# Performance work log

Hardware: AMD Instinct MI355X
Metric: run time of the kernel (lower is better)

Reference implementation:

```python
import jax, jax.numpy as jnp
import numpy as np

N = 50000
E = 800000
F_IN = 500
ID_DIM = 128
HID = 128
N_CLS = 40


def _init_linear(key, fan_in, fan_out, bias=True):
    k1, k2 = jax.random.split(key)
    bound = 1.0 / np.sqrt(fan_in)
    W = jax.random.uniform(k1, (fan_in, fan_out), minval=-bound, maxval=bound, dtype=jnp.float32)
    if bias:
        b = jax.random.uniform(k2, (fan_out,), minval=-bound, maxval=bound, dtype=jnp.float32)
        return W, b
    return W, None


def setup_inputs() -> dict:
    key = jax.random.key(0)
    ks = jax.random.split(key, 10)
    x = jax.random.normal(ks[0], (N, F_IN), dtype=jnp.float32)
    edge_index = jax.random.randint(ks[1], (2, E), 0, N, dtype=jnp.int32)
    W_map, b_map = _init_linear(ks[2], F_IN, ID_DIM)
    Wl1, bl1 = _init_linear(ks[3], ID_DIM, HID)
    Wr1, _ = _init_linear(ks[4], ID_DIM, HID, bias=False)
    Wl2, bl2 = _init_linear(ks[5], HID, 2 * HID)
    Wr2, _ = _init_linear(ks[6], HID, 2 * HID, bias=False)
    Wl3, bl3 = _init_linear(ks[7], 2 * HID, N_CLS)
    Wr3, _ = _init_linear(ks[8], 2 * HID, N_CLS, bias=False)
    return {"x": x, "edge_index": edge_index,
            "W_map": W_map, "b_map": b_map,
            "Wl1": Wl1, "bl1": bl1, "Wr1": Wr1,
            "Wl2": Wl2, "bl2": bl2, "Wr2": Wr2,
            "Wl3": Wl3, "bl3": bl3, "Wr3": Wr3}


def _sage_conv(x, src, dst, Wl, bl, Wr):
    # mean aggregation of source features into destination nodes
    agg = jax.ops.segment_sum(x[src], dst, num_segments=N)  # [N, d]
    cnt = jax.ops.segment_sum(jnp.ones((src.shape[0],), x.dtype), dst, num_segments=N)
    mean = agg / jnp.maximum(cnt, 1.0)[:, None]
    # SAGEConv (normalize=False): lin_l(mean_neigh) + lin_r(x), bias only on lin_l
    return mean @ Wl + bl + x @ Wr


def reference(x, edge_index, W_map, b_map, Wl1, bl1, Wr1, Wl2, bl2, Wr2, Wl3, bl3, Wr3):
    src, dst = edge_index[0], edge_index[1]
    h = x @ W_map + b_map                      # [N, 128]
    h = jax.nn.relu(_sage_conv(h, src, dst, Wl1, bl1, Wr1))   # dropout is identity in eval
    h = jax.nn.relu(_sage_conv(h, src, dst, Wl2, bl2, Wr2))
    h = _sage_conv(h, src, dst, Wl3, bl3, Wr3)
    return jax.nn.log_softmax(h, axis=1)
```

## Files before the change

### kernel.cpp

```cpp
#include <hip/hip_runtime.h>
#include <math.h>

#define NN 50000
#define NE 800000
#define FIN 500
#define NCLS 40
#define NB 196
#define G0 391
#define CNTB 1563
#define WSE 192512

typedef short short8 __attribute__((ext_vector_type(8)));
typedef float f32x4 __attribute__((ext_vector_type(4)));

__device__ __forceinline__ unsigned short f2bf(float f) {
    unsigned u = __float_as_uint(f);
    unsigned r = (u + 0x7FFFu + ((u >> 16) & 1u)) >> 16;
    return (unsigned short)r;
}
__device__ __forceinline__ float bf2f(unsigned short h) {
    return __uint_as_float(((unsigned)h) << 16);
}

typedef const __attribute__((address_space(1))) void gv1;
typedef __attribute__((address_space(3))) void lv3;
__device__ __forceinline__ void gl16(const void* g, void* l) {
    __builtin_amdgcn_global_load_lds((gv1*)g, (lv3*)l, 16, 0, 0);
}

__device__ __forceinline__ void wsplit_one(
    const float* __restrict__ W, short* __restrict__ dst,
    int Ksrc, int Ncols, int Kpad, int BN, int koff, int noff, int llog, int i) {
    int n = i >> llog, kk = i & ((1 << llog) - 1);
    float v = (kk < Ksrc) ? W[(size_t)kk * Ncols + n] : 0.f;
    unsigned short hi = f2bf(v);
    float lo = v - bf2f(hi);
    int nd = noff + n, kd = koff + kk;
    int yb = nd / BN, r = nd % BN;
    int ck = kd >> 6, kin = kd & 63;
    int c16h = (kin >> 3) ^ (r & 7);
    size_t rowb = (((size_t)yb * (Kpad >> 6) + ck) * BN + r) * 128;
    dst[rowb + c16h * 8 + (kin & 7)] = (short)hi;
    dst[rowb + (8 + c16h) * 8 + (kin & 7)] = (short)f2bf(lo);
}

__global__ __launch_bounds__(512) void k_mega1(
    const int* __restrict__ edst, int* __restrict__ deg,
    const float* __restrict__ W_map,
    const float* __restrict__ Wr1, const float* __restrict__ Wl1,
    const float* __restrict__ Wr2, const float* __restrict__ Wl2,
    const float* __restrict__ Wl3, const float* __restrict__ Wr3,
    short* __restrict__ m_w, short* __restrict__ b1w,
    short* __restrict__ b2w, short* __restrict__ b3w) {
    int tid = threadIdx.x;
    if (blockIdx.x < CNTB) {
        int e = blockIdx.x * 512 + tid;
        if (e < NE) atomicAdd(&deg[edst[e]], 1);
        return;
    }
    int idx = (blockIdx.x - CNTB) * 512 + tid;
    if (idx < 65536)       wsplit_one(W_map, m_w, FIN, 128, 512, 128, 0, 0, 9, idx);
    else if (idx < 81920)  wsplit_one(Wr1, b1w, 128, 128, 256, 128, 0, 0, 7, idx - 65536);
    else if (idx < 98304)  wsplit_one(Wl1, b1w, 128, 128, 256, 128, 128, 0, 7, idx - 81920);
    else if (idx < 131072) wsplit_one(Wr2, b2w, 128, 256, 256, 128, 0, 0, 7, idx - 98304);
    else if (idx < 163840) wsplit_one(Wl2, b2w, 128, 256, 256, 128, 128, 0, 7, idx - 131072);
    else if (idx < 174080) wsplit_one(Wl3, b3w, 256, 40, 256, 96, 0, 0, 8, idx - 163840);
    else if (idx < 184320) wsplit_one(Wr3, b3w, 256, 40, 256, 96, 0, 40, 8, idx - 174080);
    else if (idx < WSE) {
        int j = idx - 184320;
        int ck = j >> 11, rem = j & 2047;
        int r = 80 + (rem >> 7), c = rem & 127;
        b3w[((size_t)(ck * 96 + r)) * 128 + c] = 0;
    }
}

__global__ void k_scan1(const int* __restrict__ deg, int* __restrict__ offs,
                        int* __restrict__ bsum) {
    __shared__ int sm[256];
    int tid = threadIdx.x;
    int i = blockIdx.x * 256 + tid;
    int v = (i < NN) ? deg[i] : 0;
    sm[tid] = v;
    __syncthreads();
    for (int off = 1; off < 256; off <<= 1) {
        int t = (tid >= off) ? sm[tid - off] : 0;
        __syncthreads();
        sm[tid] += t;
        __syncthreads();
    }
    if (i < NN) offs[i] = sm[tid] - v;
    if (tid == 255) bsum[blockIdx.x] = sm[255];
}

__global__ void k_scan2(const int* __restrict__ bsum, int* __restrict__ bpre,
                        int* __restrict__ offs) {
    __shared__ int sm[256];
    int tid = threadIdx.x;
    int v = (tid < NB) ? bsum[tid] : 0;
    sm[tid] = v;
    __syncthreads();
    for (int off = 1; off < 256; off <<= 1) {
        int t = (tid >= off) ? sm[tid - off] : 0;
        __syncthreads();
        sm[tid] += t;
        __syncthreads();
    }
    if (tid < NB) bpre[tid] = sm[tid] - v;
    if (tid == 255) offs[NN] = sm[255];
}

__global__ void k_scan3(int* __restrict__ offs, const int* __restrict__ bpre,
                        int* __restrict__ cursor) {
    int i = blockIdx.x * 256 + threadIdx.x;
    if (i < NN) {
        int v = offs[i] + bpre[blockIdx.x];
        offs[i] = v;
        cursor[i] = v;
    }
}

__global__ __launch_bounds__(256) void k_aggb(
    const short* __restrict__ hb, const int* __restrict__ offs,
    const int* __restrict__ ssrc, short* __restrict__ mH) {
    int wid = (blockIdx.x * 256 + threadIdx.x) >> 6;
    int lane = threadIdx.x & 63;
    if (wid >= NN) return;
    int sub = lane >> 4, l16 = lane & 15;
    int beg = offs[wid], end = offs[wid + 1];
    f32x4 a0 = {0.f, 0.f, 0.f, 0.f}, a1 = {0.f, 0.f, 0.f, 0.f};
    for (int i = beg + sub; i < end; i += 16) {
        int i1 = i + 4, i2 = i + 8, i3 = i + 12;
        int em1 = end - 1;
        int s0 = ssrc[i];
        int s1 = ssrc[min(i1, em1)];
        int s2 = ssrc[min(i2, em1)];
        int s3 = ssrc[min(i3, em1)];
        float w1 = (i1 < end) ? 1.f : 0.f;
        float w2 = (i2 < end) ? 1.f : 0.f;
        float w3 = (i3 < end) ? 1.f : 0.f;
        short8 v0 = *(const short8*)(hb + (size_t)s0 * 128 + l16 * 8);
        short8 v1 = *(const short8*)(hb + (size_t)s1 * 128 + l16 * 8);
        short8 v2 = *(const short8*)(hb + (size_t)s2 * 128 + l16 * 8);
        short8 v3 = *(const short8*)(hb + (size_t)s3 * 128 + l16 * 8);
#pragma unroll
        for (int j = 0; j < 4; ++j) {
            a0[j] += (bf2f((unsigned short)v0[j]) + w1 * bf2f((unsigned short)v1[j])) +
                     (w2 * bf2f((unsigned short)v2[j]) + w3 * bf2f((unsigned short)v3[j]));
            a1[j] += (bf2f((unsigned short)v0[j + 4]) + w1 * bf2f((unsigned short)v1[j + 4])) +
                     (w2 * bf2f((unsigned short)v2[j + 4]) + w3 * bf2f((unsigned short)v3[j + 4]));
        }
    }
#pragma unroll
    for (int j = 0; j < 4; ++j) {
        a0[j] += __shfl_xor(a0[j], 16);
        a0[j] += __shfl_xor(a0[j], 32);
        a1[j] += __shfl_xor(a1[j], 16);
        a1[j] += __shfl_xor(a1[j], 32);
    }
    if (sub == 0) {
        float inv = 1.f / fmaxf((float)(end - beg), 1.f);
        a0 *= inv; a1 *= inv;
        short8 hv;
#pragma unroll
        for (int j = 0; j < 4; ++j) {
            hv[j] = (short)f2bf(a0[j]);
            hv[j + 4] = (short)f2bf(a1[j]);
        }
        *(short8*)(mH + (size_t)wid * 128 + l16 * 8) = hv;
    }
}

template <int BN, int KPAD, int KS0, int KREAL, bool AFP32, bool RELU, bool PQ>
__device__ __forceinline__ void gemm_body(
    const void* __restrict__ A0v, const short* __restrict__ A1,
    const short* __restrict__ Bg, const float* __restrict__ bias,
    short* __restrict__ CH, int ldc,
    float* __restrict__ F0, float* __restrict__ F1, int splitN,
    int M, int N, int bx, int by) {
    constexpr int NT = BN / 16;
    constexpr int C = KPAD / 64;
    constexpr int PT = (BN * 16) / 512;
    constexpr int SLAB = BN * 128;
    constexpr int NA = AFP32 ? 4 : 0;
    static_assert((BN * 16) % 512 == 0, "staging divisibility");
    static_assert(C >= 3, "peel structure needs >=3 chunks");
    __shared__ short Bs[2 * SLAB];
    int tid = threadIdx.x;
    int wave = tid >> 6, lane = tid & 63;
    int quad = lane >> 4, l16 = lane & 15;
    int colBase = by * BN;
    int r0 = bx * 128 + wave * 16 + l16;
    int r0c = min(r0, M - 1);
    const short* Bbase = Bg + (size_t)by * (C * SLAB);

    f32x4 acc[NT];
#pragma unroll
    for (int n = 0; n < NT; ++n) acc[n] = (f32x4){0.f, 0.f, 0.f, 0.f};

    auto stageB = [&](int buf, int ck) {
        const short* src = Bbase + (size_t)ck * SLAB;
        short* db = Bs + buf * SLAB;
#pragma unroll
        for (int u = 0; u < PT; ++u) {
            int base = u * 512 + wave * 64;
            gl16(src + (size_t)(base + lane) * 8, db + (size_t)base * 8);
        }
    };

    short8 aPre[AFP32 ? 2 : (2 * C)];
    short8 aCur[2];
    f32x4 fN[2][4];
    const float* Af = (const float*)A0v + (size_t)r0c * (size_t)KREAL;

    auto ldA32 = [&](int slot, int ck) {
#pragma unroll
        for (int s = 0; s < 2; ++s) {
            int kg = ck * 64 + s * 32 + quad * 8;
            f32x4 f0 = {0.f, 0.f, 0.f, 0.f}, f1 = {0.f, 0.f, 0.f, 0.f};
            if (kg < KREAL) f0 = *(const f32x4*)(Af + kg);
            if (kg + 4 < KREAL) f1 = *(const f32x4*)(Af + kg + 4);
            fN[slot][s * 2] = f0;
            fN[slot][s * 2 + 1] = f1;
        }
    };
    auto cvtA = [&](int slot) {
#pragma unroll
        for (int s = 0; s < 2; ++s) {
            short8 a;
#pragma unroll
            for (int j = 0; j < 4; ++j) {
                a[j] = (short)f2bf(fN[slot][s * 2][j]);
                a[j + 4] = (short)f2bf(fN[slot][s * 2 + 1][j]);
            }
            aCur[s] = a;
        }
    };
    auto compute = [&](int ck) {
        const short* bb = Bs + (ck & 1) * SLAB;
#pragma unroll
        for (int s = 0; s < 2; ++s) {
            short8 a;
            if constexpr (AFP32) a = aCur[s];
            else                 a = aPre[ck * 2 + s];
#pragma unroll
            for (int n = 0; n < NT; ++n) {
                int r = n * 16 + l16;
                int ch = (s * 4 + quad) ^ (r & 7);
                short8 bh = *(const short8*)(bb + r * 128 + ch * 8);
                short8 bl = *(const short8*)(bb + r * 128 + (8 + ch) * 8);
                acc[n] = __builtin_amdgcn_mfma_f32_16x16x32_bf16(a, bh, acc[n], 0, 0, 0);
                acc[n] = __builtin_amdgcn_mfma_f32_16x16x32_bf16(a, bl, acc[n], 0, 0, 0);
            }
        }
    };

    if constexpr (!AFP32) {
        const short* A0 = (const short*)A0v;
#pragma unroll
        for (int c = 0; c < C; ++c) {
            const bool seg = (c * 64 >= KS0);
            const short* ap = seg ? A1 : A0;
            const int w = seg ? (KPAD - KS0) : KS0;
            const int col = c * 64 - (seg ? KS0 : 0);
#pragma unroll
            for (int s = 0; s < 2; ++s)
                aPre[c * 2 + s] =
                    *(const short8*)(ap + (size_t)r0c * w + col + s * 32 + quad * 8);
        }
    }
    stageB(0, 0);
    if constexpr (AFP32) { ldA32(0, 0); ldA32(1, 1); }

#pragma unroll
    for (int ck = 0; ck <= C - 2; ++ck) {
        asm volatile("s_waitcnt vmcnt(%0)" ::"n"(NA) : "memory");
        __builtin_amdgcn_s_barrier();
        __builtin_amdgcn_sched_barrier(0);
        stageB((ck + 1) & 1, ck + 1);
        if constexpr (AFP32) {
            cvtA(ck & 1);
            if (ck + 2 < C) ldA32(ck & 1, ck + 2);
        }
        compute(ck);
    }
    {
        asm volatile("s_waitcnt vmcnt(0)" ::: "memory");
        __builtin_amdgcn_s_barrier();
        __builtin_amdgcn_sched_barrier(0);
        if constexpr (AFP32) cvtA((C - 1) & 1);
        compute(C - 1);
    }

    int gr0 = bx * 128 + wave * 16 + quad * 4;
#pragma unroll
    for (int n = 0; n < NT; ++n) {
        int gc = colBase + n * 16 + l16;
        if (gc >= N) continue;
        float b = bias ? bias[gc] : 0.f;
#pragma unroll
        for (int r = 0; r < 4; ++r) {
            int gr = gr0 + r;
            if (gr < M) {
                float v = acc[n][r] + b;
                if (RELU) v = fmaxf(v, 0.f);
                if constexpr (PQ) {
                    if (gc < splitN) CH[(size_t)gr * ldc + gc] = (short)f2bf(v);
                    else             F0[(size_t)gr * (N - splitN) + (gc - splitN)] = v;
                } else {
                    if (CH) CH[(size_t)gr * ldc + gc] = (short)f2bf(v);
                    if (F0) {
                        if (gc < splitN) F0[(size_t)gr * splitN + gc] = v;
                        else             F1[(size_t)gr * (N - splitN) + (gc - splitN)] = v;
                    }
                }
            }
        }
    }
}

template <int BN, int KPAD, int KS0, int KREAL, bool AFP32, bool RELU, bool PQ>
__global__ __launch_bounds__(512, 4) void k_mm8(
    const void* __restrict__ A0v, const short* __restrict__ A1,
    const short* __restrict__ Bg, const float* __restrict__ bias,
    short* __restrict__ CH, int ldc,
    float* __restrict__ F0, float* __restrict__ F1, int splitN,
    int M, int N) {
    gemm_body<BN, KPAD, KS0, KREAL, AFP32, RELU, PQ>(
        A0v, A1, Bg, bias, CH, ldc, F0, F1, splitN, M, N, blockIdx.x, blockIdx.y);
}

__global__ __launch_bounds__(512, 4) void k_mega2(
    const float* __restrict__ x, const short* __restrict__ m_w,
    const float* __restrict__ b_map, short* __restrict__ h0H,
    const int* __restrict__ esrc, const int* __restrict__ edst,
    int* __restrict__ cursor, int* __restrict__ ssrc) {
    if (blockIdx.x < G0) {
        gemm_body<128, 512, 512, FIN, true, false, false>(
            (const void*)x, nullptr, m_w, b_map,
            h0H, 128, nullptr, nullptr, 0, NN, 128, blockIdx.x, 0);
    } else {
        int e = (blockIdx.x - G0) * 512 + threadIdx.x;
        if (e < NE) {
            int p = atomicAdd(&cursor[edst[e]], 1);
            ssrc[p] = esrc[e];
        }
    }
}

__global__ __launch_bounds__(512, 2) void k_mm23(
    const short* __restrict__ h1H, const short* __restrict__ m1H,
    const short* __restrict__ b2w, const float* __restrict__ bl2,
    const short* __restrict__ b3w, short* __restrict__ pH,
    float* __restrict__ q) {
    constexpr int SLAB2 = 128 * 128;
    constexpr int SLAB3 = 96 * 128;
    __shared__ short Bs[2 * SLAB2];
    __shared__ short H[128 * 256];
    int tid = threadIdx.x;
    int wave = tid >> 6, lane = tid & 63;
    int quad = lane >> 4, l16 = lane & 15;
    int bx = blockIdx.x;
    int r0 = bx * 128 + wave * 16 + l16;
    int r0c = min(r0, NN - 1);

    short8 aPre[8];
#pragma unroll
    for (int c = 0; c < 4; ++c) {
        const short* ap = (c >= 2) ? m1H : h1H;
        int col = (c & 1) * 64;
#pragma unroll
        for (int s = 0; s < 2; ++s)
            aPre[c * 2 + s] =
                *(const short8*)(ap + (size_t)r0c * 128 + col + s * 32 + quad * 8);
    }

    f32x4 acc[8];
    auto compute2 = [&](int ck) {
        const short* bb = Bs + (ck & 1) * SLAB2;
#pragma unroll
        for (int s = 0; s < 2; ++s) {
            short8 a = aPre[ck * 2 + s];
#pragma unroll
            for (int n = 0; n < 8; ++n) {
                int r = n * 16 + l16;
                int ch = (s * 4 + quad) ^ (r & 7);
                short8 bh = *(const short8*)(bb + r * 128 + ch * 8);
                short8 bl = *(const short8*)(bb + r * 128 + (8 + ch) * 8);
                acc[n] = __builtin_amdgcn_mfma_f32_16x16x32_bf16(a, bh, acc[n], 0, 0, 0);
                acc[n] = __builtin_amdgcn_mfma_f32_16x16x32_bf16(a, bl, acc[n], 0, 0, 0);
            }
        }
    };

#pragma unroll
    for (int y = 0; y < 2; ++y) {
        const short* Bbase = b2w + (size_t)y * (4 * SLAB2);
        auto stageB2 = [&](int buf, int ck) {
            const short* src = Bbase + (size_t)ck * SLAB2;
            short* db = Bs + buf * SLAB2;
#pragma unroll
            for (int u = 0; u < 4; ++u) {
                int base = u * 512 + wave * 64;
                gl16(src + (size_t)(base + lane) * 8, db + (size_t)base * 8);
            }
        };
#pragma unroll
        for (int n = 0; n < 8; ++n) acc[n] = (f32x4){0.f, 0.f, 0.f, 0.f};
        stageB2(0, 0);
#pragma unroll
        for (int ck = 0; ck <= 2; ++ck) {
            asm volatile("s_waitcnt vmcnt(0)" ::: "memory");
            __builtin_amdgcn_s_barrier();
            __builtin_amdgcn_sched_barrier(0);
            stageB2((ck + 1) & 1, ck + 1);
            compute2(ck);
        }
        asm volatile("s_waitcnt vmcnt(0)" ::: "memory");
        __builtin_amdgcn_s_barrier();
        __builtin_amdgcn_sched_barrier(0);
        compute2(3);
        int lr0 = wave * 16 + quad * 4;
#pragma unroll
        for (int n = 0; n < 8; ++n) {
            int gcl = y * 128 + n * 16 + l16;
            float b = bl2[gcl];
#pragma unroll
            for (int r = 0; r < 4; ++r) {
                int lr = lr0 + r;
                int gr = bx * 128 + lr;
                float v = (gr < NN) ? fmaxf(acc[n][r] + b, 0.f) : 0.f;
                int chunk = (gcl >> 3) ^ (lr & 7);
                H[lr * 256 + chunk * 8 + (gcl & 7)] = (short)f2bf(v);
            }
        }
    }
    __syncthreads();

    auto stageB3 = [&](int buf, int ck) {
        const short* src = b3w + (size_t)ck * SLAB3;
        short* db = Bs + buf * SLAB3;
#pragma unroll
        for (int u = 0; u < 3; ++u) {
            int base = u * 512 + wave * 64;
            gl16(src + (size_t)(base + lane) * 8, db + (size_t)base * 8);
        }
    };
    stageB3(0, 0);
    int row3 = wave * 16 + l16;
    short8 aPre3[8];
#pragma unroll
    for (int c = 0; c < 4; ++c)
#pragma unroll
        for (int s = 0; s < 2; ++s) {
            int col = c * 64 + s * 32 + quad * 8;
            int chunk = (col >> 3) ^ (row3 & 7);
            aPre3[c * 2 + s] = *(const short8*)(H + row3 * 256 + chunk * 8);
        }
    f32x4 acc3[6];
#pragma unroll
    for (int n = 0; n < 6; ++n) acc3[n] = (f32x4){0.f, 0.f, 0.f, 0.f};
    auto compute3 = [&](int ck) {
        const short* bb = Bs + (ck & 1) * SLAB3;
#pragma unroll
        for (int s = 0; s < 2; ++s) {
            short8 a = aPre3[ck * 2 + s];
#pragma unroll
            for (int n = 0; n < 6; ++n) {
                int r = n * 16 + l16;
                int ch = (s * 4 + quad) ^ (r & 7);
                short8 bh = *(const short8*)(bb + r * 128 + ch * 8);
                short8 bl = *(const short8*)(bb + r * 128 + (8 + ch) * 8);
                acc3[n] = __builtin_amdgcn_mfma_f32_16x16x32_bf16(a, bh, acc3[n], 0, 0, 0);
                acc3[n] = __builtin_amdgcn_mfma_f32_16x16x32_bf16(a, bl, acc3[n], 0, 0, 0);
            }
        }
    };
#pragma unroll
    for (int ck = 0; ck <= 2; ++ck) {
        asm volatile("s_waitcnt vmcnt(0)" ::: "memory");
        __builtin_amdgcn_s_barrier();
        __builtin_amdgcn_sched_barrier(0);
        stageB3((ck + 1) & 1, ck + 1);
        compute3(ck);
    }
    asm volatile("s_waitcnt vmcnt(0)" ::: "memory");
    __builtin_amdgcn_s_barrier();
    __builtin_amdgcn_sched_barrier(0);
    compute3(3);

    int gr0 = bx * 128 + wave * 16 + quad * 4;
#pragma unroll
    for (int n = 0; n < 6; ++n) {
        int gc = n * 16 + l16;
        if (gc >= 80) continue;
#pragma unroll
        for (int r = 0; r < 4; ++r) {
            int gr = gr0 + r;
            if (gr < NN) {
                float v = acc3[n][r];
                if (gc < NCLS) pH[(size_t)gr * 64 + gc] = (short)f2bf(v);
                else           q[(size_t)gr * NCLS + (gc - NCLS)] = v;
            }
        }
    }
}

__global__ __launch_bounds__(256) void k_final(
    const short* __restrict__ pH, const float* __restrict__ q,
    const int* __restrict__ offs, const int* __restrict__ ssrc,
    const float* __restrict__ bl3, float* __restrict__ out) {
    int wid = (blockIdx.x * 256 + threadIdx.x) >> 6;
    int lane = threadIdx.x & 63;
    if (wid >= NN) return;
    bool act = lane < NCLS;
    int beg = offs[wid], end = offs[wid + 1];
    float a0 = 0.f, a1 = 0.f, a2 = 0.f, a3 = 0.f;
    for (int i = beg; i < end; i += 4) {
        int em1 = end - 1;
        int s0 = ssrc[i];
        int s1 = ssrc[min(i + 1, em1)];
        int s2 = ssrc[min(i + 2, em1)];
        int s3 = ssrc[min(i + 3, em1)];
        float w1 = (i + 1 < end) ? 1.f : 0.f;
        float w2 = (i + 2 < end) ? 1.f : 0.f;
        float w3 = (i + 3 < end) ? 1.f : 0.f;
        if (act) {
            a0 += bf2f((unsigned short)pH[(size_t)s0 * 64 + lane]);
            a1 += w1 * bf2f((unsigned short)pH[(size_t)s1 * 64 + lane]);
            a2 += w2 * bf2f((unsigned short)pH[(size_t)s2 * 64 + lane]);
            a3 += w3 * bf2f((unsigned short)pH[(size_t)s3 * 64 + lane]);
        }
    }
    float inv = 1.f / fmaxf((float)(end - beg), 1.f);
    float v = act ? ((a0 + a1) + (a2 + a3)) * inv + bl3[lane] + q[(size_t)wid * NCLS + lane]
                  : -INFINITY;
    float m = v;
#pragma unroll
    for (int off = 32; off > 0; off >>= 1) m = fmaxf(m, __shfl_xor(m, off));
    float e = act ? expf(v - m) : 0.f;
    float s = e;
#pragma unroll
    for (int off = 32; off > 0; off >>= 1) s += __shfl_xor(s, off);
    float ls = logf(s);
    if (act) out[(size_t)wid * NCLS + lane] = v - m - ls;
}

extern "C" void kernel_launch(void* const* d_in, const int* in_sizes, int n_in,
                              void* d_out, int out_size, void* d_ws, size_t ws_size,
                              hipStream_t stream) {
    const float* x    = (const float*)d_in[0];
    const int*   ei   = (const int*)d_in[1];
    const int*   esrc = ei;
    const int*   edst = ei + NE;
    const float* W_map = (const float*)d_in[2];
    const float* b_map = (const float*)d_in[3];
    const float* Wl1   = (const float*)d_in[4];
    const float* bl1   = (const float*)d_in[5];
    const float* Wr1   = (const float*)d_in[6];
    const float* Wl2   = (const float*)d_in[7];
    const float* bl2   = (const float*)d_in[8];
    const float* Wr2   = (const float*)d_in[9];
    const float* Wl3   = (const float*)d_in[10];
    const float* bl3   = (const float*)d_in[11];
    const float* Wr3   = (const float*)d_in[12];
    float* out = (float*)d_out;

    char* ws = (char*)d_ws;
    short* h0H = (short*)ws; ws += (size_t)NN * 128 * 2;
    short* m0H = (short*)ws; ws += (size_t)NN * 128 * 2;
    short* h1H = (short*)ws; ws += (size_t)NN * 128 * 2;
    short* m1H = (short*)ws; ws += (size_t)NN * 128 * 2;
    short* pH  = (short*)ws; ws += (size_t)NN * 64 * 2;
    float* q   = (float*)ws; ws += (size_t)NN * NCLS * 4;
    short* wt  = (short*)ws; ws += (size_t)376832 * 2;
    int* deg    = (int*)ws;  ws += (size_t)NN * 4;
    int* offs   = (int*)ws;  ws += (size_t)(NN + 2) * 4;
    int* cursor = (int*)ws;  ws += (size_t)NN * 4;
    int* ssrc   = (int*)ws;  ws += (size_t)NE * 4;
    int* bsum   = (int*)ws;  ws += (size_t)256 * 4;
    int* bpre   = (int*)ws;  ws += (size_t)256 * 4;

    short* m_w  = wt + 0;
    short* b1w  = wt + 131072;
    short* b2w  = wt + 196608;
    short* b3w  = wt + 327680;

    const int g128 = (NN + 127) / 128;
    const int aggBlocks = (NN * 64) / 256;
    const int wsb = (WSE + 511) / 512;

    (void)hipMemsetAsync(deg, 0, (size_t)NN * 4, stream);
    k_mega1<<<CNTB + wsb, 512, 0, stream>>>(edst, deg, W_map, Wr1, Wl1, Wr2, Wl2,
                                            Wl3, Wr3, m_w, b1w, b2w, b3w);

    k_scan1<<<NB, 256, 0, stream>>>(deg, offs, bsum);
    k_scan2<<<1, 256, 0, stream>>>(bsum, bpre, offs);
    k_scan3<<<NB, 256, 0, stream>>>(offs, bpre, cursor);

    k_mega2<<<G0 + CNTB, 512, 0, stream>>>(x, m_w, b_map, h0H, esrc, edst, cursor, ssrc);

    k_aggb<<<aggBlocks, 256, 0, stream>>>(h0H, offs, ssrc, m0H);

    k_mm8<128, 256, 128, 256, false, true, false><<<dim3(g128, 1), 512, 0, stream>>>(
        (const void*)h0H, m0H, b1w, bl1,
        h1H, 128, nullptr, nullptr, 0, NN, 128);

    k_aggb<<<aggBlocks, 256, 0, stream>>>(h1H, offs, ssrc, m1H);

    k_mm23<<<g128, 512, 0, stream>>>(h1H, m1H, b2w, bl2, b3w, pH, q);

    k_final<<<aggBlocks, 256, 0, stream>>>(pH, q, offs, ssrc, bl3, out);
}
```

Measured before the change: 403.9 us.

## Fuse neighbor mean aggregation into layer GEMM kernels, dropping m0H/m1H buffers

Removes the standalone aggregation kernels and computes each row's neighbor mean directly in the GEMM kernels' A-fragment registers, with each lane gathering its own row's neighbors. This avoids writing and rereading the mean buffers and saves two launches. The cost is less parallelism per row: one lane-quad walks all of a row's edges serially, two at a time, instead of 64 lanes splitting the edges. That may cut the gather's memory-level parallelism and stretch the GEMM prologue, and the B stage is now prefetched before the gather to overlap with it.

```diff
diff --git a/kernel.cpp b/kernel.cpp
--- a/kernel.cpp
+++ b/kernel.cpp
@@ -119,54 +119,44 @@
     }
 }
 
-__global__ __launch_bounds__(256) void k_aggb(
+__device__ __forceinline__ void agg_frag(
     const short* __restrict__ hb, const int* __restrict__ offs,
-    const int* __restrict__ ssrc, short* __restrict__ mH) {
-    int wid = (blockIdx.x * 256 + threadIdx.x) >> 6;
-    int lane = threadIdx.x & 63;
-    if (wid >= NN) return;
-    int sub = lane >> 4, l16 = lane & 15;
-    int beg = offs[wid], end = offs[wid + 1];
-    f32x4 a0 = {0.f, 0.f, 0.f, 0.f}, a1 = {0.f, 0.f, 0.f, 0.f};
-    for (int i = beg + sub; i < end; i += 16) {
-        int i1 = i + 4, i2 = i + 8, i3 = i + 12;
+    const int* __restrict__ ssrc, int row, int quad, short8* out4) {
+    int beg = offs[row], end = offs[row + 1];
+    f32x4 ac[8];
+#pragma unroll
+    for (int j = 0; j < 8; ++j) ac[j] = (f32x4){0.f, 0.f, 0.f, 0.f};
+    const short* base = hb + quad * 8;
+    for (int i = beg; i < end; i += 2) {
         int em1 = end - 1;
         int s0 = ssrc[i];
-        int s1 = ssrc[min(i1, em1)];
-        int s2 = ssrc[min(i2, em1)];
-        int s3 = ssrc[min(i3, em1)];
-        float w1 = (i1 < end) ? 1.f : 0.f;
-        float w2 = (i2 < end) ? 1.f : 0.f;
-        float w3 = (i3 < end) ? 1.f : 0.f;
-        short8 v0 = *(const short8*)(hb + (size_t)s0 * 128 + l16 * 8);
-        short8 v1 = *(const short8*)(hb + (size_t)s1 * 128 + l16 * 8);
-        short8 v2 = *(const short8*)(hb + (size_t)s2 * 128 + l16 * 8);
-        short8 v3 = *(const short8*)(hb + (size_t)s3 * 128 + l16 * 8);
+        int s1 = ssrc[min(i + 1, em1)];
+        float w1 = (i + 1 < end) ? 1.f : 0.f;
+        const short* p0 = base + (size_t)s0 * 128;
+        const short* p1 = base + (size_t)s1 * 128;
+#pragma unroll
+        for (int c4 = 0; c4 < 4; ++c4) {
+            short8 v0 = *(const short8*)(p0 + c4 * 32);
+            short8 v1 = *(const short8*)(p1 + c4 * 32);
+#pragma unroll
+            for (int j = 0; j < 4; ++j) {
+                ac[c4 * 2][j]     += bf2f((unsigned short)v0[j]) +
+                                     w1 * bf2f((unsigned short)v1[j]);
+                ac[c4 * 2 + 1][j] += bf2f((unsigned short)v0[j + 4]) +
+                                     w1 * bf2f((unsigned short)v1[j + 4]);
+            }
+        }
+    }
+    float inv = 1.f / fmaxf((float)(end - beg), 1.f);
+#pragma unroll
+    for (int c4 = 0; c4 < 4; ++c4) {
+        short8 o;
 #pragma unroll
         for (int j = 0; j < 4; ++j) {
-            a0[j] += (bf2f((unsigned short)v0[j]) + w1 * bf2f((unsigned short)v1[j])) +
-                     (w2 * bf2f((unsigned short)v2[j]) + w3 * bf2f((unsigned short)v3[j]));
-            a1[j] += (bf2f((unsigned short)v0[j + 4]) + w1 * bf2f((unsigned short)v1[j + 4])) +
-                     (w2 * bf2f((unsigned short)v2[j + 4]) + w3 * bf2f((unsigned short)v3[j + 4]));
-        }
-    }
-#pragma unroll
-    for (int j = 0; j < 4; ++j) {
-        a0[j] += __shfl_xor(a0[j], 16);
-        a0[j] += __shfl_xor(a0[j], 32);
-        a1[j] += __shfl_xor(a1[j], 16);
-        a1[j] += __shfl_xor(a1[j], 32);
-    }
-    if (sub == 0) {
-        float inv = 1.f / fmaxf((float)(end - beg), 1.f);
-        a0 *= inv; a1 *= inv;
-        short8 hv;
-#pragma unroll
-        for (int j = 0; j < 4; ++j) {
-            hv[j] = (short)f2bf(a0[j]);
-            hv[j + 4] = (short)f2bf(a1[j]);
-        }
-        *(short8*)(mH + (size_t)wid * 128 + l16 * 8) = hv;
+            o[j] = (short)f2bf(ac[c4 * 2][j] * inv);
+            o[j + 4] = (short)f2bf(ac[c4 * 2 + 1][j] * inv);
+        }
+        out4[c4] = o;
     }
 }
 
@@ -318,17 +308,6 @@
     }
 }
 
-template <int BN, int KPAD, int KS0, int KREAL, bool AFP32, bool RELU, bool PQ>
-__global__ __launch_bounds__(512, 4) void k_mm8(
-    const void* __restrict__ A0v, const short* __restrict__ A1,
-    const short* __restrict__ Bg, const float* __restrict__ bias,
-    short* __restrict__ CH, int ldc,
-    float* __restrict__ F0, float* __restrict__ F1, int splitN,
-    int M, int N) {
-    gemm_body<BN, KPAD, KS0, KREAL, AFP32, RELU, PQ>(
-        A0v, A1, Bg, bias, CH, ldc, F0, F1, splitN, M, N, blockIdx.x, blockIdx.y);
-}
-
 __global__ __launch_bounds__(512, 4) void k_mega2(
     const float* __restrict__ x, const short* __restrict__ m_w,
     const float* __restrict__ b_map, short* __restrict__ h0H,
@@ -347,11 +326,91 @@
     }
 }
 
-__global__ __launch_bounds__(512, 2) void k_mm23(
-    const short* __restrict__ h1H, const short* __restrict__ m1H,
-    const short* __restrict__ b2w, const float* __restrict__ bl2,
-    const short* __restrict__ b3w, short* __restrict__ pH,
-    float* __restrict__ q) {
+__global__ __launch_bounds__(512, 4) void k_mm1agg(
+    const short* __restrict__ h0H, const int* __restrict__ offs,
+    const int* __restrict__ ssrc, const short* __restrict__ b1w,
+    const float* __restrict__ bl1, short* __restrict__ h1H) {
+    constexpr int SLAB = 128 * 128;
+    __shared__ short Bs[2 * SLAB];
+    int tid = threadIdx.x;
+    int wave = tid >> 6, lane = tid & 63;
+    int quad = lane >> 4, l16 = lane & 15;
+    int bx = blockIdx.x;
+    int r0 = bx * 128 + wave * 16 + l16;
+    int r0c = min(r0, NN - 1);
+
+    auto stageB = [&](int buf, int ck) {
+        const short* src = b1w + (size_t)ck * SLAB;
+        short* db = Bs + buf * SLAB;
+#pragma unroll
+        for (int u = 0; u < 4; ++u) {
+            int base = u * 512 + wave * 64;
+            gl16(src + (size_t)(base + lane) * 8, db + (size_t)base * 8);
+        }
+    };
+    stageB(0, 0);
+
+    short8 aPre[8];
+#pragma unroll
+    for (int c = 0; c < 2; ++c)
+#pragma unroll
+        for (int s = 0; s < 2; ++s)
+            aPre[c * 2 + s] =
+                *(const short8*)(h0H + (size_t)r0c * 128 + c * 64 + s * 32 + quad * 8);
+    agg_frag(h0H, offs, ssrc, r0c, quad, &aPre[4]);
+
+    f32x4 acc[8];
+#pragma unroll
+    for (int n = 0; n < 8; ++n) acc[n] = (f32x4){0.f, 0.f, 0.f, 0.f};
+    auto compute = [&](int ck) {
+        const short* bb = Bs + (ck & 1) * SLAB;
+#pragma unroll
+        for (int s = 0; s < 2; ++s) {
+            short8 a = aPre[ck * 2 + s];
+#pragma unroll
+            for (int n = 0; n < 8; ++n) {
+                int r = n * 16 + l16;
+                int ch = (s * 4 + quad) ^ (r & 7);
+                short8 bh = *(const short8*)(bb + r * 128 + ch * 8);
+                short8 bl = *(const short8*)(bb + r * 128 + (8 + ch) * 8);
+                acc[n] = __builtin_amdgcn_mfma_f32_16x16x32_bf16(a, bh, acc[n], 0, 0, 0);
+                acc[n] = __builtin_amdgcn_mfma_f32_16x16x32_bf16(a, bl, acc[n], 0, 0, 0);
+            }
+        }
+    };
+
+#pragma unroll
+    for (int ck = 0; ck <= 2; ++ck) {
+        asm volatile("s_waitcnt vmcnt(0)" ::: "memory");
+        __builtin_amdgcn_s_barrier();
+        __builtin_amdgcn_sched_barrier(0);
+        stageB((ck + 1) & 1, ck + 1);
+        compute(ck);
+    }
+    asm volatile("s_waitcnt vmcnt(0)" ::: "memory");
+    __builtin_amdgcn_s_barrier();
+    __builtin_amdgcn_sched_barrier(0);
+    compute(3);
+
+    int gr0 = bx * 128 + wave * 16 + quad * 4;
+#pragma unroll
+    for (int n = 0; n < 8; ++n) {
+        int gc = n * 16 + l16;
+        float b = bl1[gc];
+#pragma unroll
+        for (int r = 0; r < 4; ++r) {
+            int gr = gr0 + r;
+            if (gr < NN)
+                h1H[(size_t)gr * 128 + gc] = (short)f2bf(fmaxf(acc[n][r] + b, 0.f));
+        }
+    }
+}
+
+__global__ __launch_bounds__(512, 2) void k_mm23agg(
+    const short* __restrict__ h1H, const int* __restrict__ offs,
+    const int* __restrict__ ssrc, const short* __restrict__ b2w,
+    const float* __restrict__ bl2, const short* __restrict__ b3w,
+    short* __restrict__ pH, float* __restrict__ q) {
     constexpr int SLAB2 = 128 * 128;
     constexpr int SLAB3 = 96 * 128;
     __shared__ short Bs[2 * SLAB2];
@@ -363,16 +422,23 @@
     int r0 = bx * 128 + wave * 16 + l16;
     int r0c = min(r0, NN - 1);
 
+    {
+        const short* src = b2w;
+#pragma unroll
+        for (int u = 0; u < 4; ++u) {
+            int base = u * 512 + wave * 64;
+            gl16(src + (size_t)(base + lane) * 8, Bs + (size_t)base * 8);
+        }
+    }
+
     short8 aPre[8];
 #pragma unroll
-    for (int c = 0; c < 4; ++c) {
-        const short* ap = (c >= 2) ? m1H : h1H;
-        int col = (c & 1) * 64;
+    for (int c = 0; c < 2; ++c)
 #pragma unroll
         for (int s = 0; s < 2; ++s)
             aPre[c * 2 + s] =
-                *(const short8*)(ap + (size_t)r0c * 128 + col + s * 32 + quad * 8);
-    }
+                *(const short8*)(h1H + (size_t)r0c * 128 + c * 64 + s * 32 + quad * 8);
+    agg_frag(h1H, offs, ssrc, r0c, quad, &aPre[4]);
 
     f32x4 acc[8];
     auto compute2 = [&](int ck) {
@@ -406,7 +472,7 @@
         };
 #pragma unroll
         for (int n = 0; n < 8; ++n) acc[n] = (f32x4){0.f, 0.f, 0.f, 0.f};
-        stageB2(0, 0);
+        if (y == 1) stageB2(0, 0);
 #pragma unroll
         for (int ck = 0; ck <= 2; ++ck) {
             asm volatile("s_waitcnt vmcnt(0)" ::: "memory");
@@ -567,9 +633,7 @@
 
     char* ws = (char*)d_ws;
     short* h0H = (short*)ws; ws += (size_t)NN * 128 * 2;
-    short* m0H = (short*)ws; ws += (size_t)NN * 128 * 2;
     short* h1H = (short*)ws; ws += (size_t)NN * 128 * 2;
-    short* m1H = (short*)ws; ws += (size_t)NN * 128 * 2;
     short* pH  = (short*)ws; ws += (size_t)NN * 64 * 2;
     float* q   = (float*)ws; ws += (size_t)NN * NCLS * 4;
     short* wt  = (short*)ws; ws += (size_t)376832 * 2;
@@ -599,15 +663,9 @@
 
     k_mega2<<<G0 + CNTB, 512, 0, stream>>>(x, m_w, b_map, h0H, esrc, edst, cursor, ssrc);
 
-    k_aggb<<<aggBlocks, 256, 0, stream>>>(h0H, offs, ssrc, m0H);
-
-    k_mm8<128, 256, 128, 256, false, true, false><<<dim3(g128, 1), 512, 0, stream>>>(
-        (const void*)h0H, m0H, b1w, bl1,
-        h1H, 128, nullptr, nullptr, 0, NN, 128);
-
-    k_aggb<<<aggBlocks, 256, 0, stream>>>(h1H, offs, ssrc, m1H);
-
-    k_mm23<<<g128, 512, 0, stream>>>(h1H, m1H, b2w, bl2, b3w, pH, q);
+    k_mm1agg<<<g128, 512, 0, stream>>>(h0H, offs, ssrc, b1w, bl1, h1H);
+
+    k_mm23agg<<<g128, 512, 0, stream>>>(h1H, offs, ssrc, b2w, bl2, b3w, pH, q);
 
     k_final<<<aggBlocks, 256, 0, stream>>>(pH, q, offs, ssrc, bl3, out);
 }
```

New measurement: 430.9 us. 1.07x slower.
